# Kernel optimization log

Hardware: AMD Instinct MI355X
Metric: run time of the kernel (lower is better)

## Reference

```python
import jax, jax.numpy as jnp
import numpy as np


def setup_inputs() -> dict:
    key = jax.random.key(0)
    k1, k2, k3 = jax.random.split(key, 3)
    B, C, H, W, K = 8, 256, 128, 128, 19
    feature = jax.random.normal(k1, (B, C, H, W), dtype=jnp.float32)
    map_ = jax.random.uniform(k2, (B, K, H, W), dtype=jnp.float32)
    # nn.Parameter, shape (1,1,1,1,K); original inits to zeros, use small randn
    # so the output is non-trivial for kernel correctness checking.
    gamma = jax.random.normal(k3, (1, 1, 1, 1, K), dtype=jnp.float32) * 0.1
    return {"feature": feature, "map": map_, "gamma": gamma}


def reference(feature, map, gamma):
    # Original: for each class k, att[b,c] = sum_hw feature[b,c,h,w]*map[b,k,h,w],
    # out_k = sigmoid(att)[...,None,None] * feature; result = feature + sum_k out_k*gamma[k].
    # Collapse per-class loop into one batched contraction + fused gate-reduce.
    att = jnp.einsum('bchw,bkhw->bck', feature, map)          # [B,C,K]
    scale = jnp.einsum('bck,k->bc', jax.nn.sigmoid(att), gamma.reshape(-1))  # [B,C]
    return feature + feature * scale[:, :, None, None]
```

## Files before the change

kernel.cpp:

```cpp
#include <hip/hip_runtime.h>
#include <math.h>

#define BB 8
#define CC 256
#define KK 19
#define HW 16384
#define HW4 4096

#define CHUNK4 32
#define NS (HW4 / CHUNK4)

#define FOR_K(OP) OP(0) OP(1) OP(2) OP(3) OP(4) OP(5) OP(6) OP(7) OP(8) OP(9) \
                  OP(10) OP(11) OP(12) OP(13) OP(14) OP(15) OP(16) OP(17) OP(18)

__global__ __launch_bounds__(256, 4) void CGM_k1_contract(
    const float* __restrict__ feature,
    const float* __restrict__ map_,
    float* __restrict__ att,
    float* __restrict__ part)
{
    const int bI = blockIdx.x;
    const int s  = bI & (NS - 1);
    const int b  = bI >> 7;
    const int c  = threadIdx.x;

    __shared__ float4 mlds[KK * CHUNK4];

    const float4* m4 = (const float4*)map_ + (size_t)b * KK * HW4 + s * CHUNK4;
    for (int idx = threadIdx.x; idx < KK * CHUNK4; idx += 256) {
        const int k = idx >> 5;
        const int j = idx & 31;
        mlds[idx] = m4[(size_t)k * HW4 + j];
    }
    __syncthreads();

    float acc[KK];
#define ZERO(K) acc[K] = 0.f;
    FOR_K(ZERO)
#undef ZERO

    const float4* f4 = (const float4*)feature
                     + (size_t)(b * CC + c) * HW4 + s * CHUNK4;

    for (int g = 0; g < 4; ++g) {
        float4 f[8];
#pragma unroll
        for (int u = 0; u < 8; ++u) f[u] = f4[g * 8 + u];
#pragma unroll
        for (int u = 0; u < 8; ++u) {
            const int i = g * 8 + u;
            const float4 fv = f[u];
#define STEP(K) { const float4 m = mlds[(K) * CHUNK4 + i]; \
                  acc[K] += fv.x * m.x + fv.y * m.y + fv.z * m.z + fv.w * m.w; }
            FOR_K(STEP)
#undef STEP
        }
    }

    if (part) {
        float* dst = part + (size_t)bI * (KK * CC) + c;
#define FIN(K) dst[(K) * CC] = acc[K];
        FOR_K(FIN)
#undef FIN
    } else {
        float* dst = att + (size_t)(b * CC + c) * KK;
#define FIN(K) atomicAdd(&dst[K], acc[K]);
        FOR_K(FIN)
#undef FIN
    }
}

__global__ __launch_bounds__(256) void CGM_k1b_reduce(
    const float* __restrict__ part,
    float* __restrict__ att)
{
    const int bk = blockIdx.x;
    const int b  = bk / KK;
    const int k  = bk - b * KK;
    const int c  = threadIdx.x;

    const float* p = part + ((size_t)(b * NS) * KK + k) * CC + c;
    float s0 = 0.f, s1 = 0.f, s2 = 0.f, s3 = 0.f;
#pragma unroll 4
    for (int s = 0; s < NS; s += 4) {
        s0 += p[(size_t)(s + 0) * KK * CC];
        s1 += p[(size_t)(s + 1) * KK * CC];
        s2 += p[(size_t)(s + 2) * KK * CC];
        s3 += p[(size_t)(s + 3) * KK * CC];
    }
    att[(size_t)(b * CC + c) * KK + k] = (s0 + s1) + (s2 + s3);
}

#define S2 8
#define CT2 16
#define CHUNK24 (HW4 / S2)

__global__ __launch_bounds__(256) void CGM_k2_apply(
    const float* __restrict__ feature,
    const float* __restrict__ gamma,
    const float* __restrict__ att,
    float* __restrict__ out)
{
    const int bI = blockIdx.x;
    const int ct = bI & 15;
    const int s  = (bI >> 4) & (S2 - 1);
    const int b  = bI >> 7;
    const int t  = threadIdx.x;
    const int c0 = ct * CT2;

    __shared__ float sgk[CT2 * KK];
    __shared__ float scale[CT2];

    for (int idx = t; idx < CT2 * KK; idx += 256) {
        const int c = idx / KK;
        const int k = idx - c * KK;
        const float a = att[(size_t)(b * CC + c0 + c) * KK + k];
        const float sig = 1.f / (1.f + __expf(-a));
        sgk[idx] = sig * gamma[k];
    }
    __syncthreads();

    if (t < CT2) {
        float ssum = 0.f;
#define ADDK(K) ssum += sgk[t * KK + (K)];
        FOR_K(ADDK)
#undef ADDK
        scale[t] = 1.f + ssum;
    }
    __syncthreads();

    const float4* f4 = (const float4*)feature + (size_t)(b * CC + c0) * HW4;
    float4*       o4 = (float4*)out           + (size_t)(b * CC + c0) * HW4;
    const int ibase = s * CHUNK24;
#pragma unroll
    for (int c = 0; c < CT2; ++c) {
        const float sc = scale[c];
#pragma unroll
        for (int r = 0; r < CHUNK24 / 256; ++r) {
            const int i = ibase + r * 256 + t;
            const float4 f = f4[(size_t)c * HW4 + i];
            float4 o;
            o.x = f.x * sc;
            o.y = f.y * sc;
            o.z = f.z * sc;
            o.w = f.w * sc;
            o4[(size_t)c * HW4 + i] = o;
        }
    }
}

extern "C" void kernel_launch(void* const* d_in, const int* in_sizes, int n_in,
                              void* d_out, int out_size, void* d_ws, size_t ws_size,
                              hipStream_t stream) {
    const float* feature = (const float*)d_in[0];
    const float* map_    = (const float*)d_in[1];
    const float* gamma   = (const float*)d_in[2];
    float* out           = (float*)d_out;
    float* att           = (float*)d_ws;

    const size_t att_bytes  = (size_t)BB * CC * KK * sizeof(float);
    const size_t part_off   = (att_bytes + 255) & ~(size_t)255;
    const size_t part_bytes = (size_t)BB * NS * KK * CC * sizeof(float);
    const bool   split      = ws_size >= part_off + part_bytes;
    float* part = split ? (float*)((char*)d_ws + part_off) : nullptr;

    if (!split) {
        hipMemsetAsync(att, 0, att_bytes, stream);
    }

    const int grid1 = BB * NS;
    CGM_k1_contract<<<grid1, 256, 0, stream>>>(feature, map_, att, part);

    if (split) {
        CGM_k1b_reduce<<<BB * KK, 256, 0, stream>>>(part, att);
    }

    const int grid2 = BB * S2 * (CC / CT2);
    CGM_k2_apply<<<grid2, 256, 0, stream>>>(feature, gamma, att, out);
}
```

Before: 311.3 us.

## Register-block two channels per thread in contraction and vectorize partial reduction

Each thread in the contraction kernel now accumulates two channels (c and c+128) over half of the spatial chunk, so every map value read from LDS feeds two channels. The two halves are combined through shared memory at the end. The partial buffer layout is changed to [K][B][NS][C], which lets the reduce kernel read float4s contiguously and split the NS sum across four wave groups combined in LDS. This doubles accumulator register pressure to 38 floats and adds an extra LDS reduction step.

```diff
diff --git a/kernel.cpp b/kernel.cpp
--- a/kernel.cpp
+++ b/kernel.cpp
@@ -22,51 +22,71 @@
     const int bI = blockIdx.x;
     const int s  = bI & (NS - 1);
     const int b  = bI >> 7;
-    const int c  = threadIdx.x;
-
-    __shared__ float4 mlds[KK * CHUNK4];
+    const int t  = threadIdx.x;
+    const int c  = t & 127;
+    const int h  = t >> 7;
+
+    __shared__ float smem[KK * 2 * 128];
+    float4* mlds = (float4*)smem;
 
     const float4* m4 = (const float4*)map_ + (size_t)b * KK * HW4 + s * CHUNK4;
-    for (int idx = threadIdx.x; idx < KK * CHUNK4; idx += 256) {
+    for (int idx = t; idx < KK * CHUNK4; idx += 256) {
         const int k = idx >> 5;
         const int j = idx & 31;
         mlds[idx] = m4[(size_t)k * HW4 + j];
     }
     __syncthreads();
 
-    float acc[KK];
-#define ZERO(K) acc[K] = 0.f;
+    float accA[KK], accB[KK];
+#define ZERO(K) accA[K] = 0.f; accB[K] = 0.f;
     FOR_K(ZERO)
 #undef ZERO
 
-    const float4* f4 = (const float4*)feature
-                     + (size_t)(b * CC + c) * HW4 + s * CHUNK4;
-
+    const float4* fA = (const float4*)feature
+                     + (size_t)(b * CC + c) * HW4 + s * CHUNK4 + h * 16;
+    const float4* fB = fA + (size_t)128 * HW4;
+
+#pragma unroll 1
     for (int g = 0; g < 4; ++g) {
-        float4 f[8];
-#pragma unroll
-        for (int u = 0; u < 8; ++u) f[u] = f4[g * 8 + u];
-#pragma unroll
-        for (int u = 0; u < 8; ++u) {
-            const int i = g * 8 + u;
-            const float4 fv = f[u];
+        float4 fa[4], fb[4];
+#pragma unroll
+        for (int u = 0; u < 4; ++u) { fa[u] = fA[g * 4 + u]; fb[u] = fB[g * 4 + u]; }
+#pragma unroll
+        for (int u = 0; u < 4; ++u) {
+            const int i = h * 16 + g * 4 + u;
+            const float4 av = fa[u];
+            const float4 bv = fb[u];
 #define STEP(K) { const float4 m = mlds[(K) * CHUNK4 + i]; \
-                  acc[K] += fv.x * m.x + fv.y * m.y + fv.z * m.z + fv.w * m.w; }
+                  accA[K] += av.x * m.x + av.y * m.y + av.z * m.z + av.w * m.w; \
+                  accB[K] += bv.x * m.x + bv.y * m.y + bv.z * m.z + bv.w * m.w; }
             FOR_K(STEP)
 #undef STEP
         }
     }
 
-    if (part) {
-        float* dst = part + (size_t)bI * (KK * CC) + c;
-#define FIN(K) dst[(K) * CC] = acc[K];
-        FOR_K(FIN)
+    __syncthreads();
+    if (h == 1) {
+#define SPILL(K) { smem[(K) * 256 + c] = accA[K]; smem[(K) * 256 + 128 + c] = accB[K]; }
+        FOR_K(SPILL)
+#undef SPILL
+    }
+    __syncthreads();
+    if (h == 0) {
+        if (part) {
+#define FIN(K) { const float s0 = accA[K] + smem[(K) * 256 + c]; \
+                 const float s1 = accB[K] + smem[(K) * 256 + 128 + c]; \
+                 float* d = part + ((size_t)((K) * BB + b) * NS + s) * CC; \
+                 d[c] = s0; d[c + 128] = s1; }
+            FOR_K(FIN)
 #undef FIN
-    } else {
-        float* dst = att + (size_t)(b * CC + c) * KK;
-#define FIN(K) atomicAdd(&dst[K], acc[K]);
-        FOR_K(FIN)
+        } else {
+#define FIN(K) { const float s0 = accA[K] + smem[(K) * 256 + c]; \
+                 const float s1 = accB[K] + smem[(K) * 256 + 128 + c]; \
+                 atomicAdd(&att[(size_t)(b * CC + c) * KK + (K)], s0); \
+                 atomicAdd(&att[(size_t)(b * CC + c + 128) * KK + (K)], s1); }
+            FOR_K(FIN)
 #undef FIN
+        }
     }
 }
 
@@ -77,18 +97,47 @@
     const int bk = blockIdx.x;
     const int b  = bk / KK;
     const int k  = bk - b * KK;
-    const int c  = threadIdx.x;
-
-    const float* p = part + ((size_t)(b * NS) * KK + k) * CC + c;
-    float s0 = 0.f, s1 = 0.f, s2 = 0.f, s3 = 0.f;
-#pragma unroll 4
-    for (int s = 0; s < NS; s += 4) {
-        s0 += p[(size_t)(s + 0) * KK * CC];
-        s1 += p[(size_t)(s + 1) * KK * CC];
-        s2 += p[(size_t)(s + 2) * KK * CC];
-        s3 += p[(size_t)(s + 3) * KK * CC];
-    }
-    att[(size_t)(b * CC + c) * KK + k] = (s0 + s1) + (s2 + s3);
+    const int t  = threadIdx.x;
+    const int q  = t & 63;
+    const int sg = t >> 6;
+
+    const float4* p4 = (const float4*)(part + (size_t)(k * BB + b) * NS * CC)
+                     + (size_t)(sg * 32) * 64 + q;
+
+    float4 a0 = {0.f, 0.f, 0.f, 0.f}, a1 = a0, a2 = a0, a3 = a0;
+#pragma unroll 2
+    for (int i = 0; i < 32; i += 4) {
+        const float4 v0 = p4[(size_t)(i + 0) * 64];
+        const float4 v1 = p4[(size_t)(i + 1) * 64];
+        const float4 v2 = p4[(size_t)(i + 2) * 64];
+        const float4 v3 = p4[(size_t)(i + 3) * 64];
+        a0.x += v0.x; a0.y += v0.y; a0.z += v0.z; a0.w += v0.w;
+        a1.x += v1.x; a1.y += v1.y; a1.z += v1.z; a1.w += v1.w;
+        a2.x += v2.x; a2.y += v2.y; a2.z += v2.z; a2.w += v2.w;
+        a3.x += v3.x; a3.y += v3.y; a3.z += v3.z; a3.w += v3.w;
+    }
+    float4 r;
+    r.x = (a0.x + a1.x) + (a2.x + a3.x);
+    r.y = (a0.y + a1.y) + (a2.y + a3.y);
+    r.z = (a0.z + a1.z) + (a2.z + a3.z);
+    r.w = (a0.w + a1.w) + (a2.w + a3.w);
+
+    __shared__ float4 red[4][64];
+    red[sg][q] = r;
+    __syncthreads();
+    if (t < 64) {
+        const float4 u0 = red[0][q], u1 = red[1][q], u2 = red[2][q], u3 = red[3][q];
+        float4 o;
+        o.x = (u0.x + u1.x) + (u2.x + u3.x);
+        o.y = (u0.y + u1.y) + (u2.y + u3.y);
+        o.z = (u0.z + u1.z) + (u2.z + u3.z);
+        o.w = (u0.w + u1.w) + (u2.w + u3.w);
+        float* d = att + ((size_t)b * CC + 4 * q) * KK + k;
+        d[0 * KK] = o.x;
+        d[1 * KK] = o.y;
+        d[2 * KK] = o.z;
+        d[3 * KK] = o.w;
+    }
 }
 
 #define S2 8
@@ -160,7 +209,7 @@
 
     const size_t att_bytes  = (size_t)BB * CC * KK * sizeof(float);
     const size_t part_off   = (att_bytes + 255) & ~(size_t)255;
-    const size_t part_bytes = (size_t)BB * NS * KK * CC * sizeof(float);
+    const size_t part_bytes = (size_t)KK * BB * NS * CC * sizeof(float);
     const bool   split      = ws_size >= part_off + part_bytes;
     float* part = split ? (float*)((char*)d_ws + part_off) : nullptr;
 
```

New measurement: 1.000 ms. 221% more time.

## Restructure contraction kernel into register-tiled 4-channel by 5-class wave blocks

Applied to the files above, without the earlier changes.

The contraction kernel drops the shared-memory staging of map tiles. Each wave now computes a 4-channel by 5-class register tile directly from global loads over a quarter of the spatial extent. Partial sums are laid out per (class, batch, channel) with 256 spatial partials each, and the reduce kernel reads them with float4 loads. This targets the LDS-bandwidth bottleneck of the old inner loop, but re-reads the map once per channel group and doubles the partial-sum buffer written and read.

```diff
diff --git a/kernel.cpp b/kernel.cpp
--- a/kernel.cpp
+++ b/kernel.cpp
@@ -7,66 +7,87 @@
 #define HW 16384
 #define HW4 4096
 
-#define CHUNK4 32
-#define NS (HW4 / CHUNK4)
+
+typedef float f32x4 __attribute__((ext_vector_type(4)));
 
 #define FOR_K(OP) OP(0) OP(1) OP(2) OP(3) OP(4) OP(5) OP(6) OP(7) OP(8) OP(9) \
                   OP(10) OP(11) OP(12) OP(13) OP(14) OP(15) OP(16) OP(17) OP(18)
 
-__global__ __launch_bounds__(256, 4) void CGM_k1_contract(
+#define DOT(A, M, F) A += M.x * F.x + M.y * F.y + M.z * F.z + M.w * F.w;
+
+__global__ __launch_bounds__(256) void CGM_k1_contract(
     const float* __restrict__ feature,
     const float* __restrict__ map_,
     float* __restrict__ att,
     float* __restrict__ part)
 {
     const int bI = blockIdx.x;
-    const int s  = bI & (NS - 1);
-    const int b  = bI >> 7;
-    const int c  = threadIdx.x;
-
-    __shared__ float4 mlds[KK * CHUNK4];
-
-    const float4* m4 = (const float4*)map_ + (size_t)b * KK * HW4 + s * CHUNK4;
-    for (int idx = threadIdx.x; idx < KK * CHUNK4; idx += 256) {
-        const int k = idx >> 5;
-        const int j = idx & 31;
-        mlds[idx] = m4[(size_t)k * HW4 + j];
-    }
-    __syncthreads();
-
-    float acc[KK];
-#define ZERO(K) acc[K] = 0.f;
-    FOR_K(ZERO)
-#undef ZERO
-
-    const float4* f4 = (const float4*)feature
-                     + (size_t)(b * CC + c) * HW4 + s * CHUNK4;
-
-    for (int g = 0; g < 4; ++g) {
-        float4 f[8];
-#pragma unroll
-        for (int u = 0; u < 8; ++u) f[u] = f4[g * 8 + u];
-#pragma unroll
-        for (int u = 0; u < 8; ++u) {
-            const int i = g * 8 + u;
-            const float4 fv = f[u];
-#define STEP(K) { const float4 m = mlds[(K) * CHUNK4 + i]; \
-                  acc[K] += fv.x * m.x + fv.y * m.y + fv.z * m.z + fv.w * m.w; }
-            FOR_K(STEP)
-#undef STEP
-        }
-    }
-
+    const int cg = bI & 63;
+    const int sh = (bI >> 6) & 3;
+    const int b  = bI >> 8;
+    const int t  = threadIdx.x;
+    const int l  = t & 63;
+    const int w  = t >> 6;
+
+    const int klo = w * 5;
+    const size_t k4row = (size_t)((w == 3) ? 3 : 4) * HW4;
+
+    const float4* mb = (const float4*)map_
+                     + ((size_t)b * KK + klo) * HW4 + sh * 1024 + l;
+    const float4* fb = (const float4*)feature
+                     + ((size_t)b * CC + cg * 4) * HW4 + sh * 1024 + l;
+
+    float a00 = 0.f, a01 = 0.f, a02 = 0.f, a03 = 0.f, a04 = 0.f;
+    float a10 = 0.f, a11 = 0.f, a12 = 0.f, a13 = 0.f, a14 = 0.f;
+    float a20 = 0.f, a21 = 0.f, a22 = 0.f, a23 = 0.f, a24 = 0.f;
+    float a30 = 0.f, a31 = 0.f, a32 = 0.f, a33 = 0.f, a34 = 0.f;
+
+#pragma unroll 1
+    for (int u = 0; u < 16; ++u) {
+        const int off = u * 64;
+        const float4 m0 = mb[off];
+        const float4 m1 = mb[off + 1 * HW4];
+        const float4 m2 = mb[off + 2 * HW4];
+        const float4 m3 = mb[off + 3 * HW4];
+        const float4 m4 = mb[off + k4row];
+        const float4 f0 = fb[off];
+        const float4 f1 = fb[off + 1 * HW4];
+        const float4 f2 = fb[off + 2 * HW4];
+        const float4 f3 = fb[off + 3 * HW4];
+        DOT(a00, m0, f0) DOT(a01, m1, f0) DOT(a02, m2, f0)
+        DOT(a03, m3, f0) DOT(a04, m4, f0)
+        DOT(a10, m0, f1) DOT(a11, m1, f1) DOT(a12, m2, f1)
+        DOT(a13, m3, f1) DOT(a14, m4, f1)
+        DOT(a20, m0, f2) DOT(a21, m1, f2) DOT(a22, m2, f2)
+        DOT(a23, m3, f2) DOT(a24, m4, f2)
+        DOT(a30, m0, f3) DOT(a31, m1, f3) DOT(a32, m2, f3)
+        DOT(a33, m3, f3) DOT(a34, m4, f3)
+    }
+
+    const int c0 = cg * 4;
+    const int e  = sh * 64 + l;
     if (part) {
-        float* dst = part + (size_t)bI * (KK * CC) + c;
-#define FIN(K) dst[(K) * CC] = acc[K];
-        FOR_K(FIN)
-#undef FIN
+#define STK(KI, V0, V1, V2, V3) if (klo + (KI) < KK) {                   \
+        float* d = part + (((size_t)(klo + (KI)) * BB + b) * CC + c0) * 256 + e; \
+        d[0 * 256] = V0; d[1 * 256] = V1; d[2 * 256] = V2; d[3 * 256] = V3; }
+        STK(0, a00, a10, a20, a30)
+        STK(1, a01, a11, a21, a31)
+        STK(2, a02, a12, a22, a32)
+        STK(3, a03, a13, a23, a33)
+        STK(4, a04, a14, a24, a34)
+#undef STK
     } else {
-        float* dst = att + (size_t)(b * CC + c) * KK;
-#define FIN(K) atomicAdd(&dst[K], acc[K]);
-        FOR_K(FIN)
-#undef FIN
+#define STK(KI, V0, V1, V2, V3) if (klo + (KI) < KK) {                   \
+        atomicAdd(&att[(size_t)(b * CC + c0 + 0) * KK + klo + (KI)], V0); \
+        atomicAdd(&att[(size_t)(b * CC + c0 + 1) * KK + klo + (KI)], V1); \
+        atomicAdd(&att[(size_t)(b * CC + c0 + 2) * KK + klo + (KI)], V2); \
+        atomicAdd(&att[(size_t)(b * CC + c0 + 3) * KK + klo + (KI)], V3); }
+        STK(0, a00, a10, a20, a30)
+        STK(1, a01, a11, a21, a31)
+        STK(2, a02, a12, a22, a32)
+        STK(3, a03, a13, a23, a33)
+        STK(4, a04, a14, a24, a34)
+#undef STK
     }
 }
 
@@ -77,18 +98,28 @@
     const int bk = blockIdx.x;
     const int b  = bk / KK;
     const int k  = bk - b * KK;
-    const int c  = threadIdx.x;
-
-    const float* p = part + ((size_t)(b * NS) * KK + k) * CC + c;
-    float s0 = 0.f, s1 = 0.f, s2 = 0.f, s3 = 0.f;
+    const int t  = threadIdx.x;
+
+    const float4* p4 = (const float4*)(part
+                     + (((size_t)k * BB + b) * CC + t) * 256);
+
+    float4 a0 = {0.f, 0.f, 0.f, 0.f}, a1 = a0, a2 = a0, a3 = a0;
 #pragma unroll 4
-    for (int s = 0; s < NS; s += 4) {
-        s0 += p[(size_t)(s + 0) * KK * CC];
-        s1 += p[(size_t)(s + 1) * KK * CC];
-        s2 += p[(size_t)(s + 2) * KK * CC];
-        s3 += p[(size_t)(s + 3) * KK * CC];
-    }
-    att[(size_t)(b * CC + c) * KK + k] = (s0 + s1) + (s2 + s3);
+    for (int i = 0; i < 64; i += 4) {
+        const float4 v0 = p4[i + 0];
+        const float4 v1 = p4[i + 1];
+        const float4 v2 = p4[i + 2];
+        const float4 v3 = p4[i + 3];
+        a0.x += v0.x; a0.y += v0.y; a0.z += v0.z; a0.w += v0.w;
+        a1.x += v1.x; a1.y += v1.y; a1.z += v1.z; a1.w += v1.w;
+        a2.x += v2.x; a2.y += v2.y; a2.z += v2.z; a2.w += v2.w;
+        a3.x += v3.x; a3.y += v3.y; a3.z += v3.z; a3.w += v3.w;
+    }
+    const float sx = (a0.x + a1.x) + (a2.x + a3.x);
+    const float sy = (a0.y + a1.y) + (a2.y + a3.y);
+    const float sz = (a0.z + a1.z) + (a2.z + a3.z);
+    const float sw = (a0.w + a1.w) + (a2.w + a3.w);
+    att[(size_t)(b * CC + t) * KK + k] = (sx + sy) + (sz + sw);
 }
 
 #define S2 8
@@ -160,7 +191,7 @@
 
     const size_t att_bytes  = (size_t)BB * CC * KK * sizeof(float);
     const size_t part_off   = (att_bytes + 255) & ~(size_t)255;
-    const size_t part_bytes = (size_t)BB * NS * KK * CC * sizeof(float);
+    const size_t part_bytes = (size_t)KK * BB * CC * 256 * sizeof(float);
     const bool   split      = ws_size >= part_off + part_bytes;
     float* part = split ? (float*)((char*)d_ws + part_off) : nullptr;
 
@@ -168,7 +199,7 @@
         hipMemsetAsync(att, 0, att_bytes, stream);
     }
 
-    const int grid1 = BB * NS;
+    const int grid1 = BB * 4 * 64;
     CGM_k1_contract<<<grid1, 256, 0, stream>>>(feature, map_, att, part);
 
     if (split) {
```

After: 311.7 us. Within noise of the previous version (+0.1%).
